# Optimization experiments

Measured on AMD Instinct MI355X. Metric: run time of the kernel, lower is better.

## Reference

```python
import jax, jax.numpy as jnp
import numpy as np

N_NODES = 50000
N_EDGES = 800000
H_DIM = 128
N_REL = 40
N_BASES = 4


def setup_inputs() -> dict:
    key = jax.random.key(0)
    ks = jax.random.split(key, 9)
    h = jax.random.normal(ks[0], (N_NODES, H_DIM), jnp.float32)
    norm = jax.random.uniform(ks[1], (N_EDGES, 1), jnp.float32)
    basis_w = jax.random.normal(ks[2], (N_BASES, H_DIM, H_DIM), jnp.float32) * 0.05
    w_comp = jax.random.normal(ks[3], (N_REL, N_BASES), jnp.float32) * 0.5
    loop_w = jax.random.normal(ks[4], (H_DIM, H_DIM), jnp.float32) * 0.05
    bias = jax.random.normal(ks[5], (H_DIM,), jnp.float32) * 0.05
    src = jax.random.randint(ks[6], (N_EDGES,), 0, N_NODES, jnp.int32)
    dst = jax.random.randint(ks[7], (N_EDGES,), 0, N_NODES, jnp.int32)
    etype = jax.random.randint(ks[8], (N_EDGES,), 0, N_REL, jnp.int32)
    return {"h": h, "norm": norm, "basis_w": basis_w, "w_comp": w_comp,
            "loop_w": loop_w, "bias": bias, "src": src, "dst": dst, "etype": etype}


def reference(h, norm, basis_w, w_comp, loop_w, bias, src, dst, etype):
    # RelGraphConv with 'basis' regularizer, one layer (num_hidden_layers=1):
    #   W_r = sum_b w_comp[r, b] * basis_w[b]
    #   m_e = (h[src_e] @ W_{etype_e}) * norm_e
    #   agg[v] = sum_{e: dst_e = v} m_e
    #   out = relu(agg + bias + h @ loop_w)   (dropout = 0)
    # Contraction reordered for memory efficiency: scatter-add per-basis
    # scaled source features first (node-level), then apply small basis GEMMs.
    n = h.shape[0]
    n_bases = basis_w.shape[0]
    coeff = w_comp[etype] * norm          # [E, B] per-edge basis coefficients * norm
    h_src = h[src]                        # [E, D] edge-gathered source features
    agg = jnp.zeros((n, basis_w.shape[2]), dtype=h.dtype)
    for b in range(n_bases):              # small fixed loop over bases
        s_b = jax.ops.segment_sum(coeff[:, b:b + 1] * h_src, dst, num_segments=n)  # [N, D]
        agg = agg + s_b @ basis_w[b]
    return jax.nn.relu(agg + bias + h @ loop_w)
```

## Files before the change

### kernel.cpp

```cpp
#include <hip/hip_runtime.h>
#include <hip/hip_bf16.h>
#include <stdint.h>

#define N_NODES 50000
#define N_EDGES 800000
#define H_DIM 128
#define N_REL 40
#define N_BASES 4
#define A_COLS 640
#define N_RANGES 196
#define EP_BLOCKS 200
#define EDGES_PER_BLK 4000
#define STAGE_CAP 5120

typedef __attribute__((ext_vector_type(8))) short bf16x8;
typedef __attribute__((ext_vector_type(4))) float f32x4;

__device__ __forceinline__ unsigned short f2bf(float f) {
    unsigned int u = __float_as_uint(f);
    unsigned int r = u + 0x7fffu + ((u >> 16) & 1u);
    return (unsigned short)(r >> 16);
}

__global__ __launch_bounds__(256) void prep_kernel(
        const float* __restrict__ h,
        const float* __restrict__ basis_w, const float* __restrict__ loop_w,
        const int* __restrict__ src, const int* __restrict__ dst,
        const int* __restrict__ etype, const float* __restrict__ norm,
        unsigned short* __restrict__ A, unsigned short* __restrict__ wt3,
        uint2* __restrict__ pkd, int* __restrict__ gcnt) {
    int bid = blockIdx.x;
    if (bid < 3125) {
        int t = bid * 256 + threadIdx.x;
        int row = t >> 4;
        int cb = (t & 15) * 8;
        const float* p = h + (size_t)row * 128 + cb;
        float4 a0 = ((const float4*)p)[0];
        float4 a1 = ((const float4*)p)[1];
        bf16x8 o;
        o[0] = (short)f2bf(a0.x); o[1] = (short)f2bf(a0.y);
        o[2] = (short)f2bf(a0.z); o[3] = (short)f2bf(a0.w);
        o[4] = (short)f2bf(a1.x); o[5] = (short)f2bf(a1.y);
        o[6] = (short)f2bf(a1.z); o[7] = (short)f2bf(a1.w);
        *(bf16x8*)(A + (size_t)row * A_COLS + cb) = o;
    } else if (bid < 3130) {
        int mat = bid - 3125;
        const float* srcm = (mat < 4) ? (basis_w + mat * 16384) : loop_w;
        int koff = (mat < 4) ? (128 + mat * 128) : 0;
        int t = threadIdx.x;
#pragma unroll
        for (int i = 0; i < 16; ++i) {
            int f = t + i * 256;
            int k = f >> 5;
            int j4 = (f & 31) * 4;
            float4 v = ((const float4*)srcm)[f];
            int kg = koff + k;
            int ks = kg >> 5;
            int quad = (kg >> 3) & 3;
            int jj = kg & 7;
            float vv[4] = {v.x, v.y, v.z, v.w};
#pragma unroll
            for (int d = 0; d < 4; ++d) {
                int j = j4 + d;
                int cg = j >> 4;
                int n16 = j & 15;
                wt3[(size_t)((ks * 8 + cg) * 64 + quad * 16 + n16) * 8 + jj] =
                    f2bf(vv[d]);
            }
        }
    } else {
        __shared__ int lhist[N_RANGES];
        int blk = bid - 3130;
        int t = threadIdx.x;
        if (t < N_RANGES) lhist[t] = 0;
        __syncthreads();
        int e0 = blk * EDGES_PER_BLK;
        for (int i = t; i < EDGES_PER_BLK; i += 256) {
            int e = e0 + i;
            int d = dst[e];
            unsigned int nbf = f2bf(norm[e]);
            pkd[e] = make_uint2((unsigned)src[e] | ((unsigned)etype[e] << 20),
                                (unsigned)d | (nbf << 17));
            atomicAdd(&lhist[d >> 8], 1);
        }
        __syncthreads();
        if (t < N_RANGES) gcnt[t * EP_BLOCKS + blk] = lhist[t];
    }
}

__global__ __launch_bounds__(256) void bucket_scan_a(
        const int* __restrict__ gcnt, int* __restrict__ blkbase,
        int* __restrict__ btot) {
    __shared__ int wsum[4];
    int r = blockIdx.x;
    int t = threadIdx.x, lane = t & 63, w = t >> 6;
    int x = (t < EP_BLOCKS) ? gcnt[r * EP_BLOCKS + t] : 0;
    int v = x;
#pragma unroll
    for (int d = 1; d < 64; d <<= 1) {
        int y = __shfl_up(v, d);
        if (lane >= d) v += y;
    }
    if (lane == 63) wsum[w] = v;
    __syncthreads();
    int wpre = 0;
    if (w > 0) wpre += wsum[0];
    if (w > 1) wpre += wsum[1];
    if (w > 2) wpre += wsum[2];
    if (t < EP_BLOCKS) blkbase[r * EP_BLOCKS + t] = wpre + v - x;
    if (t == 255) btot[r] = wpre + v;
}

__global__ __launch_bounds__(256) void bucket_scan_b(
        const int* __restrict__ btot, int* __restrict__ bstart,
        int* __restrict__ offs) {
    __shared__ int wsum[4];
    int t = threadIdx.x, lane = t & 63, w = t >> 6;
    int x = (t < N_RANGES) ? btot[t] : 0;
    int v = x;
#pragma unroll
    for (int d = 1; d < 64; d <<= 1) {
        int y = __shfl_up(v, d);
        if (lane >= d) v += y;
    }
    if (lane == 63) wsum[w] = v;
    __syncthreads();
    int wpre = 0;
    if (w > 0) wpre += wsum[0];
    if (w > 1) wpre += wsum[1];
    if (w > 2) wpre += wsum[2];
    if (t < N_RANGES) bstart[t] = wpre + v - x;
    if (t == 255) {
        bstart[N_RANGES] = wpre + v;
        offs[N_NODES] = wpre + v;
    }
}

__global__ __launch_bounds__(256) void binscatter(
        const uint2* __restrict__ pkd, const int* __restrict__ blkbase,
        const int* __restrict__ bstart, uint2* __restrict__ bucketed) {
    __shared__ int lcur[N_RANGES];
    int t = threadIdx.x;
    if (t < N_RANGES)
        lcur[t] = bstart[t] + blkbase[t * EP_BLOCKS + blockIdx.x];
    __syncthreads();
    int e0 = blockIdx.x * EDGES_PER_BLK;
    for (int i = t; i < EDGES_PER_BLK; i += 256) {
        uint2 p = pkd[e0 + i];
        int r = (p.y & 0x1FFFF) >> 8;
        int pos = atomicAdd(&lcur[r], 1);
        bucketed[pos] = p;
    }
}

__global__ __launch_bounds__(256) void bucket_sort(
        const int* __restrict__ bstart, const uint2* __restrict__ bucketed,
        uint2* __restrict__ sorted_pe, int* __restrict__ offs) {
    __shared__ int hist[256];
    __shared__ int cur[256];
    __shared__ int wsum[4];
    __shared__ uint2 stage[STAGE_CAP];
    int r = blockIdx.x;
    int t = threadIdx.x, lane = t & 63, w = t >> 6;
    int begin = bstart[r];
    int end = bstart[r + 1];
    int n = end - begin;
    hist[t] = 0;
    __syncthreads();
    for (int i = begin + t; i < end; i += 256)
        atomicAdd(&hist[bucketed[i].y & 255], 1);
    __syncthreads();
    int x = hist[t];
    int v = x;
#pragma unroll
    for (int d = 1; d < 64; d <<= 1) {
        int y = __shfl_up(v, d);
        if (lane >= d) v += y;
    }
    if (lane == 63) wsum[w] = v;
    __syncthreads();
    int wpre = 0;
    if (w > 0) wpre += wsum[0];
    if (w > 1) wpre += wsum[1];
    if (w > 2) wpre += wsum[2];
    int excl_rel = wpre + v - x;
    int node = r * 256 + t;
    if (node < N_NODES) offs[node] = begin + excl_rel;
    cur[t] = excl_rel;
    __syncthreads();
    if (n <= STAGE_CAP) {
        for (int i = begin + t; i < end; i += 256) {
            uint2 p = bucketed[i];
            int pos = atomicAdd(&cur[p.y & 255], 1);
            stage[pos] = make_uint2(p.x, (p.y >> 17) << 16);
        }
        __syncthreads();
        for (int i = t; i < n; i += 256)
            sorted_pe[begin + i] = stage[i];
    } else {
        for (int i = begin + t; i < end; i += 256) {
            uint2 p = bucketed[i];
            int pos = atomicAdd(&cur[p.y & 255], 1);
            sorted_pe[begin + pos] = make_uint2(p.x, (p.y >> 17) << 16);
        }
    }
}

__global__ __launch_bounds__(256) void aggregate_kernel(
        const int* __restrict__ offs, const uint2* __restrict__ sorted_pe,
        const float* __restrict__ w_comp,
        unsigned short* __restrict__ A) {
    int v = __builtin_amdgcn_readfirstlane(blockIdx.x * 4 + (threadIdx.x >> 6));
    if (v >= N_NODES) return;
    int lane = threadIdx.x & 63;
    int begin = offs[v];
    int end = offs[v + 1];

    float a0l = 0.f, a0h = 0.f, a1l = 0.f, a1h = 0.f;
    float a2l = 0.f, a2h = 0.f, a3l = 0.f, a3h = 0.f;

    const unsigned int* Au = (const unsigned int*)A;

    int j = begin;
    for (; j + 8 <= end; j += 8) {
        uint2 p[8];
        unsigned int u[8];
#pragma unroll
        for (int q = 0; q < 8; ++q) p[q] = sorted_pe[j + q];
#pragma unroll
        for (int q = 0; q < 8; ++q)
            u[q] = Au[(size_t)(p[q].x & 0xFFFFF) * 320 + lane];
#pragma unroll
        for (int q = 0; q < 8; ++q) {
            float4 wc = ((const float4*)w_comp)[p[q].x >> 20];
            float nm = __uint_as_float(p[q].y);
            float lo = __uint_as_float(u[q] << 16);
            float hi = __uint_as_float(u[q] & 0xffff0000u);
            a0l += (wc.x * nm) * lo; a0h += (wc.x * nm) * hi;
            a1l += (wc.y * nm) * lo; a1h += (wc.y * nm) * hi;
            a2l += (wc.z * nm) * lo; a2h += (wc.z * nm) * hi;
            a3l += (wc.w * nm) * lo; a3h += (wc.w * nm) * hi;
        }
    }
    for (; j < end; ++j) {
        uint2 p = sorted_pe[j];
        int s = p.x & 0xFFFFF;
        float4 wc = ((const float4*)w_comp)[p.x >> 20];
        float nm = __uint_as_float(p.y);
        unsigned int u = Au[(size_t)s * 320 + lane];
        float lo = __uint_as_float(u << 16);
        float hi = __uint_as_float(u & 0xffff0000u);
        a0l += (wc.x * nm) * lo; a0h += (wc.x * nm) * hi;
        a1l += (wc.y * nm) * lo; a1h += (wc.y * nm) * hi;
        a2l += (wc.z * nm) * lo; a2h += (wc.z * nm) * hi;
        a3l += (wc.w * nm) * lo; a3h += (wc.w * nm) * hi;
    }

    unsigned int* ps = (unsigned int*)(A + (size_t)v * A_COLS + 128);
    ps[0 * 64 + lane] = (unsigned int)f2bf(a0l) | ((unsigned int)f2bf(a0h) << 16);
    ps[1 * 64 + lane] = (unsigned int)f2bf(a1l) | ((unsigned int)f2bf(a1h) << 16);
    ps[2 * 64 + lane] = (unsigned int)f2bf(a2l) | ((unsigned int)f2bf(a2h) << 16);
    ps[3 * 64 + lane] = (unsigned int)f2bf(a3l) | ((unsigned int)f2bf(a3h) << 16);
}

__global__ __launch_bounds__(256, 2) void gemm_out(
        const unsigned short* __restrict__ A,
        const unsigned short* __restrict__ wt3,
        const float* __restrict__ bias,
        float* __restrict__ out) {
    int wv = threadIdx.x >> 6;
    int lane = threadIdx.x & 63;
    int n16 = lane & 15;
    int quad = lane >> 4;
    int r0 = (blockIdx.x * 4 + wv) * 32;

    const unsigned short* ap0 = A + (size_t)(r0 + n16) * A_COLS + quad * 8;
    const unsigned short* ap1 = ap0 + 16 * A_COLS;
    const unsigned short* bp = wt3 + (size_t)lane * 8;

    f32x4 acc[2][8];
#pragma unroll
    for (int rt = 0; rt < 2; ++rt)
#pragma unroll
        for (int ct = 0; ct < 8; ++ct)
            acc[rt][ct] = (f32x4)0.f;

    bf16x8 a_cur[2], b_cur[8];
    a_cur[0] = *(const bf16x8*)ap0;
    a_cur[1] = *(const bf16x8*)ap1;
#pragma unroll
    for (int ct = 0; ct < 8; ++ct)
        b_cur[ct] = *(const bf16x8*)(bp + ct * 512);

#pragma unroll
    for (int ks = 0; ks < 20; ++ks) {
        bf16x8 a_nxt[2], b_nxt[8];
        if (ks < 19) {
            a_nxt[0] = *(const bf16x8*)(ap0 + (ks + 1) * 32);
            a_nxt[1] = *(const bf16x8*)(ap1 + (ks + 1) * 32);
#pragma unroll
            for (int ct = 0; ct < 8; ++ct)
                b_nxt[ct] = *(const bf16x8*)(bp + (ks + 1) * 4096 + ct * 512);
        } else {
            a_nxt[0] = a_cur[0];
            a_nxt[1] = a_cur[1];
#pragma unroll
            for (int ct = 0; ct < 8; ++ct) b_nxt[ct] = b_cur[ct];
        }
#pragma unroll
        for (int ct = 0; ct < 8; ++ct) {
            acc[0][ct] = __builtin_amdgcn_mfma_f32_16x16x32_bf16(a_cur[0], b_cur[ct], acc[0][ct], 0, 0, 0);
            acc[1][ct] = __builtin_amdgcn_mfma_f32_16x16x32_bf16(a_cur[1], b_cur[ct], acc[1][ct], 0, 0, 0);
        }
        a_cur[0] = a_nxt[0];
        a_cur[1] = a_nxt[1];
#pragma unroll
        for (int ct = 0; ct < 8; ++ct) b_cur[ct] = b_nxt[ct];
    }

#pragma unroll
    for (int rt = 0; rt < 2; ++rt) {
        int rbase = r0 + rt * 16 + quad * 4;
#pragma unroll
        for (int ct = 0; ct < 8; ++ct) {
            int col = ct * 16 + n16;
            float bv = bias[col];
#pragma unroll
            for (int rg = 0; rg < 4; ++rg) {
                int r = rbase + rg;
                if (r < N_NODES)
                    out[(size_t)r * H_DIM + col] = fmaxf(acc[rt][ct][rg] + bv, 0.f);
            }
        }
    }
}

extern "C" void kernel_launch(void* const* d_in, const int* in_sizes, int n_in,
                              void* d_out, int out_size, void* d_ws, size_t ws_size,
                              hipStream_t stream) {
    const float* h       = (const float*)d_in[0];
    const float* norm    = (const float*)d_in[1];
    const float* basis_w = (const float*)d_in[2];
    const float* w_comp  = (const float*)d_in[3];
    const float* loop_w  = (const float*)d_in[4];
    const float* bias    = (const float*)d_in[5];
    const int*   src     = (const int*)d_in[6];
    const int*   dst     = (const int*)d_in[7];
    const int*   etype   = (const int*)d_in[8];
    float* out = (float*)d_out;

    char* base = (char*)d_ws;
    unsigned short* wt3       = (unsigned short*)(base + 0);
    unsigned short* A         = (unsigned short*)(base + 163840);
    int*            offs      = (int*)(base + 64225280);
    uint2*          pkd       = (uint2*)(base + 64425344);
    uint2*          bucketed  = (uint2*)(base + 70825344);
    uint2*          sorted_pe = (uint2*)(base + 77225344);
    int*            gcnt      = (int*)(base + 83625344);
    int*            blkbase   = (int*)(base + 83782144);
    int*            bstart    = (int*)(base + 83938944);
    int*            btot      = (int*)(base + 83939732);

    prep_kernel<<<3330, 256, 0, stream>>>(h, basis_w, loop_w,
                                          src, dst, etype, norm,
                                          A, wt3, pkd, gcnt);
    bucket_scan_a<<<N_RANGES, 256, 0, stream>>>(gcnt, blkbase, btot);
    bucket_scan_b<<<1, 256, 0, stream>>>(btot, bstart, offs);
    binscatter<<<EP_BLOCKS, 256, 0, stream>>>(pkd, blkbase, bstart, bucketed);
    bucket_sort<<<N_RANGES, 256, 0, stream>>>(bstart, bucketed, sorted_pe, offs);
    aggregate_kernel<<<12500, 256, 0, stream>>>(offs, sorted_pe, w_comp, A);
    gemm_out<<<391, 256, 0, stream>>>(A, wt3, bias, out);
}
```

Baseline: 199.2 us.

## Fuse aggregation into output GEMM via shared memory and fold bucket scan into consumers

Fuses the per-node aggregation kernel with the output GEMM. Each block aggregates 32 nodes into a swizzled LDS tile that feeds MFMA directly, so the 640-column bf16 intermediate is no longer written to and read back from global memory. The bf16 copy of h shrinks to 128 columns, and the single-block global scan is recomputed redundantly inside binscatter and bucket_sort, which removes two launches. The cost is 40KB of LDS per block, which lowers occupancy, and a per-block aggregation phase whose load imbalance can stall the MFMA phase.

```diff
diff --git a/kernel.cpp b/kernel.cpp
--- a/kernel.cpp
+++ b/kernel.cpp
@@ -1,5 +1,4 @@
 #include <hip/hip_runtime.h>
-#include <hip/hip_bf16.h>
 #include <stdint.h>
 
 #define N_NODES 50000
@@ -7,7 +6,6 @@
 #define H_DIM 128
 #define N_REL 40
 #define N_BASES 4
-#define A_COLS 640
 #define N_RANGES 196
 #define EP_BLOCKS 200
 #define EDGES_PER_BLK 4000
@@ -42,7 +40,7 @@
         o[2] = (short)f2bf(a0.z); o[3] = (short)f2bf(a0.w);
         o[4] = (short)f2bf(a1.x); o[5] = (short)f2bf(a1.y);
         o[6] = (short)f2bf(a1.z); o[7] = (short)f2bf(a1.w);
-        *(bf16x8*)(A + (size_t)row * A_COLS + cb) = o;
+        *(bf16x8*)(A + (size_t)row * H_DIM + cb) = o;
     } else if (bid < 3130) {
         int mat = bid - 3125;
         const float* srcm = (mat < 4) ? (basis_w + mat * 16384) : loop_w;
@@ -111,9 +109,10 @@
     if (t == 255) btot[r] = wpre + v;
 }
 
-__global__ __launch_bounds__(256) void bucket_scan_b(
-        const int* __restrict__ btot, int* __restrict__ bstart,
-        int* __restrict__ offs) {
+__global__ __launch_bounds__(256) void binscatter(
+        const uint2* __restrict__ pkd, const int* __restrict__ blkbase,
+        const int* __restrict__ btot, uint2* __restrict__ bucketed) {
+    __shared__ int lcur[N_RANGES];
     __shared__ int wsum[4];
     int t = threadIdx.x, lane = t & 63, w = t >> 6;
     int x = (t < N_RANGES) ? btot[t] : 0;
@@ -129,20 +128,8 @@
     if (w > 0) wpre += wsum[0];
     if (w > 1) wpre += wsum[1];
     if (w > 2) wpre += wsum[2];
-    if (t < N_RANGES) bstart[t] = wpre + v - x;
-    if (t == 255) {
-        bstart[N_RANGES] = wpre + v;
-        offs[N_NODES] = wpre + v;
-    }
-}
-
-__global__ __launch_bounds__(256) void binscatter(
-        const uint2* __restrict__ pkd, const int* __restrict__ blkbase,
-        const int* __restrict__ bstart, uint2* __restrict__ bucketed) {
-    __shared__ int lcur[N_RANGES];
-    int t = threadIdx.x;
     if (t < N_RANGES)
-        lcur[t] = bstart[t] + blkbase[t * EP_BLOCKS + blockIdx.x];
+        lcur[t] = (wpre + v - x) + blkbase[t * EP_BLOCKS + blockIdx.x];
     __syncthreads();
     int e0 = blockIdx.x * EDGES_PER_BLK;
     for (int i = t; i < EDGES_PER_BLK; i += 256) {
@@ -154,23 +141,16 @@
 }
 
 __global__ __launch_bounds__(256) void bucket_sort(
-        const int* __restrict__ bstart, const uint2* __restrict__ bucketed,
+        const int* __restrict__ btot, const uint2* __restrict__ bucketed,
         uint2* __restrict__ sorted_pe, int* __restrict__ offs) {
     __shared__ int hist[256];
     __shared__ int cur[256];
     __shared__ int wsum[4];
+    __shared__ int sbeg;
     __shared__ uint2 stage[STAGE_CAP];
     int r = blockIdx.x;
     int t = threadIdx.x, lane = t & 63, w = t >> 6;
-    int begin = bstart[r];
-    int end = bstart[r + 1];
-    int n = end - begin;
-    hist[t] = 0;
-    __syncthreads();
-    for (int i = begin + t; i < end; i += 256)
-        atomicAdd(&hist[bucketed[i].y & 255], 1);
-    __syncthreads();
-    int x = hist[t];
+    int x = (t < N_RANGES) ? btot[t] : 0;
     int v = x;
 #pragma unroll
     for (int d = 1; d < 64; d <<= 1) {
@@ -178,14 +158,37 @@
         if (lane >= d) v += y;
     }
     if (lane == 63) wsum[w] = v;
+    hist[t] = 0;
     __syncthreads();
     int wpre = 0;
     if (w > 0) wpre += wsum[0];
     if (w > 1) wpre += wsum[1];
     if (w > 2) wpre += wsum[2];
-    int excl_rel = wpre + v - x;
+    if (t == r) sbeg = wpre + v - x;
+    __syncthreads();
+    int begin = sbeg;
+    int end = begin + btot[r];
+    int n = end - begin;
+    for (int i = begin + t; i < end; i += 256)
+        atomicAdd(&hist[bucketed[i].y & 255], 1);
+    __syncthreads();
+    int x2 = hist[t];
+    int v2 = x2;
+#pragma unroll
+    for (int d = 1; d < 64; d <<= 1) {
+        int y = __shfl_up(v2, d);
+        if (lane >= d) v2 += y;
+    }
+    if (lane == 63) wsum[w] = v2;
+    __syncthreads();
+    int wpre2 = 0;
+    if (w > 0) wpre2 += wsum[0];
+    if (w > 1) wpre2 += wsum[1];
+    if (w > 2) wpre2 += wsum[2];
+    int excl_rel = wpre2 + v2 - x2;
     int node = r * 256 + t;
     if (node < N_NODES) offs[node] = begin + excl_rel;
+    if (r == N_RANGES - 1 && t == 0) offs[N_NODES] = N_EDGES;
     cur[t] = excl_rel;
     __syncthreads();
     if (n <= STAGE_CAP) {
@@ -206,130 +209,113 @@
     }
 }
 
-__global__ __launch_bounds__(256) void aggregate_kernel(
+__global__ __launch_bounds__(256) void agg_gemm(
         const int* __restrict__ offs, const uint2* __restrict__ sorted_pe,
         const float* __restrict__ w_comp,
-        unsigned short* __restrict__ A) {
-    int v = __builtin_amdgcn_readfirstlane(blockIdx.x * 4 + (threadIdx.x >> 6));
-    if (v >= N_NODES) return;
-    int lane = threadIdx.x & 63;
-    int begin = offs[v];
-    int end = offs[v + 1];
-
-    float a0l = 0.f, a0h = 0.f, a1l = 0.f, a1h = 0.f;
-    float a2l = 0.f, a2h = 0.f, a3l = 0.f, a3h = 0.f;
-
-    const unsigned int* Au = (const unsigned int*)A;
-
-    int j = begin;
-    for (; j + 8 <= end; j += 8) {
-        uint2 p[8];
-        unsigned int u[8];
-#pragma unroll
-        for (int q = 0; q < 8; ++q) p[q] = sorted_pe[j + q];
-#pragma unroll
-        for (int q = 0; q < 8; ++q)
-            u[q] = Au[(size_t)(p[q].x & 0xFFFFF) * 320 + lane];
-#pragma unroll
-        for (int q = 0; q < 8; ++q) {
-            float4 wc = ((const float4*)w_comp)[p[q].x >> 20];
-            float nm = __uint_as_float(p[q].y);
-            float lo = __uint_as_float(u[q] << 16);
-            float hi = __uint_as_float(u[q] & 0xffff0000u);
-            a0l += (wc.x * nm) * lo; a0h += (wc.x * nm) * hi;
-            a1l += (wc.y * nm) * lo; a1h += (wc.y * nm) * hi;
-            a2l += (wc.z * nm) * lo; a2h += (wc.z * nm) * hi;
-            a3l += (wc.w * nm) * lo; a3h += (wc.w * nm) * hi;
-        }
-    }
-    for (; j < end; ++j) {
-        uint2 p = sorted_pe[j];
-        int s = p.x & 0xFFFFF;
-        float4 wc = ((const float4*)w_comp)[p.x >> 20];
-        float nm = __uint_as_float(p.y);
-        unsigned int u = Au[(size_t)s * 320 + lane];
-        float lo = __uint_as_float(u << 16);
-        float hi = __uint_as_float(u & 0xffff0000u);
-        a0l += (wc.x * nm) * lo; a0h += (wc.x * nm) * hi;
-        a1l += (wc.y * nm) * lo; a1h += (wc.y * nm) * hi;
-        a2l += (wc.z * nm) * lo; a2h += (wc.z * nm) * hi;
-        a3l += (wc.w * nm) * lo; a3h += (wc.w * nm) * hi;
-    }
-
-    unsigned int* ps = (unsigned int*)(A + (size_t)v * A_COLS + 128);
-    ps[0 * 64 + lane] = (unsigned int)f2bf(a0l) | ((unsigned int)f2bf(a0h) << 16);
-    ps[1 * 64 + lane] = (unsigned int)f2bf(a1l) | ((unsigned int)f2bf(a1h) << 16);
-    ps[2 * 64 + lane] = (unsigned int)f2bf(a2l) | ((unsigned int)f2bf(a2h) << 16);
-    ps[3 * 64 + lane] = (unsigned int)f2bf(a3l) | ((unsigned int)f2bf(a3h) << 16);
-}
-
-__global__ __launch_bounds__(256, 2) void gemm_out(
-        const unsigned short* __restrict__ A,
+        const unsigned short* __restrict__ Ab,
         const unsigned short* __restrict__ wt3,
-        const float* __restrict__ bias,
-        float* __restrict__ out) {
+        const float* __restrict__ bias, float* __restrict__ out) {
+    __shared__ __align__(16) unsigned short S[32 * 640];
     int wv = threadIdx.x >> 6;
     int lane = threadIdx.x & 63;
+    int nbase = blockIdx.x * 32;
+    const unsigned int* Au = (const unsigned int*)Ab;
+
+    for (int q = 0; q < 8; ++q) {
+        int row = (wv << 3) + q;
+        int v = __builtin_amdgcn_readfirstlane(nbase + row);
+        float a0l = 0.f, a0h = 0.f, a1l = 0.f, a1h = 0.f;
+        float a2l = 0.f, a2h = 0.f, a3l = 0.f, a3h = 0.f;
+        unsigned int hb = 0u;
+        if (v < N_NODES) {
+            hb = Au[(size_t)v * 64 + lane];
+            int begin = offs[v];
+            int end = offs[v + 1];
+            int j = begin;
+            for (; j + 8 <= end; j += 8) {
+                uint2 p[8];
+                unsigned int u[8];
+#pragma unroll
+                for (int k = 0; k < 8; ++k) p[k] = sorted_pe[j + k];
+#pragma unroll
+                for (int k = 0; k < 8; ++k)
+                    u[k] = Au[(size_t)(p[k].x & 0xFFFFF) * 64 + lane];
+#pragma unroll
+                for (int k = 0; k < 8; ++k) {
+                    float4 wc = ((const float4*)w_comp)[p[k].x >> 20];
+                    float nm = __uint_as_float(p[k].y);
+                    float lo = __uint_as_float(u[k] << 16);
+                    float hi = __uint_as_float(u[k] & 0xffff0000u);
+                    a0l += (wc.x * nm) * lo; a0h += (wc.x * nm) * hi;
+                    a1l += (wc.y * nm) * lo; a1h += (wc.y * nm) * hi;
+                    a2l += (wc.z * nm) * lo; a2h += (wc.z * nm) * hi;
+                    a3l += (wc.w * nm) * lo; a3h += (wc.w * nm) * hi;
+                }
+            }
+            for (; j < end; ++j) {
+                uint2 p = sorted_pe[j];
+                float4 wc = ((const float4*)w_comp)[p.x >> 20];
+                float nm = __uint_as_float(p.y);
+                unsigned int u = Au[(size_t)(p.x & 0xFFFFF) * 64 + lane];
+                float lo = __uint_as_float(u << 16);
+                float hi = __uint_as_float(u & 0xffff0000u);
+                a0l += (wc.x * nm) * lo; a0h += (wc.x * nm) * hi;
+                a1l += (wc.y * nm) * lo; a1h += (wc.y * nm) * hi;
+                a2l += (wc.z * nm) * lo; a2h += (wc.z * nm) * hi;
+                a3l += (wc.w * nm) * lo; a3h += (wc.w * nm) * hi;
+            }
+        }
+        char* rp = (char*)S + row * 1280;
+        int swz = (row & 7) << 4;
+        *(unsigned int*)(rp + ((lane * 4) ^ swz)) = hb;
+        *(unsigned int*)(rp + ((256 + lane * 4) ^ swz)) =
+            (unsigned int)f2bf(a0l) | ((unsigned int)f2bf(a0h) << 16);
+        *(unsigned int*)(rp + ((512 + lane * 4) ^ swz)) =
+            (unsigned int)f2bf(a1l) | ((unsigned int)f2bf(a1h) << 16);
+        *(unsigned int*)(rp + ((768 + lane * 4) ^ swz)) =
+            (unsigned int)f2bf(a2l) | ((unsigned int)f2bf(a2h) << 16);
+        *(unsigned int*)(rp + ((1024 + lane * 4) ^ swz)) =
+            (unsigned int)f2bf(a3l) | ((unsigned int)f2bf(a3h) << 16);
+    }
+    __syncthreads();
+
     int n16 = lane & 15;
     int quad = lane >> 4;
-    int r0 = (blockIdx.x * 4 + wv) * 32;
-
-    const unsigned short* ap0 = A + (size_t)(r0 + n16) * A_COLS + quad * 8;
-    const unsigned short* ap1 = ap0 + 16 * A_COLS;
-    const unsigned short* bp = wt3 + (size_t)lane * 8;
-
-    f32x4 acc[2][8];
+    f32x4 acc[2][2];
 #pragma unroll
     for (int rt = 0; rt < 2; ++rt)
 #pragma unroll
-        for (int ct = 0; ct < 8; ++ct)
-            acc[rt][ct] = (f32x4)0.f;
-
-    bf16x8 a_cur[2], b_cur[8];
-    a_cur[0] = *(const bf16x8*)ap0;
-    a_cur[1] = *(const bf16x8*)ap1;
-#pragma unroll
-    for (int ct = 0; ct < 8; ++ct)
-        b_cur[ct] = *(const bf16x8*)(bp + ct * 512);
+        for (int c = 0; c < 2; ++c) acc[rt][c] = (f32x4)0.f;
+
+    const char* a0p = (const char*)S + n16 * 1280;
+    const char* a1p = (const char*)S + (16 + n16) * 1280;
+    int swz2 = (n16 & 7) << 4;
+    const unsigned short* bp = wt3 + (size_t)(wv * 2) * 512 + lane * 8;
 
 #pragma unroll
     for (int ks = 0; ks < 20; ++ks) {
-        bf16x8 a_nxt[2], b_nxt[8];
-        if (ks < 19) {
-            a_nxt[0] = *(const bf16x8*)(ap0 + (ks + 1) * 32);
-            a_nxt[1] = *(const bf16x8*)(ap1 + (ks + 1) * 32);
-#pragma unroll
-            for (int ct = 0; ct < 8; ++ct)
-                b_nxt[ct] = *(const bf16x8*)(bp + (ks + 1) * 4096 + ct * 512);
-        } else {
-            a_nxt[0] = a_cur[0];
-            a_nxt[1] = a_cur[1];
-#pragma unroll
-            for (int ct = 0; ct < 8; ++ct) b_nxt[ct] = b_cur[ct];
-        }
-#pragma unroll
-        for (int ct = 0; ct < 8; ++ct) {
-            acc[0][ct] = __builtin_amdgcn_mfma_f32_16x16x32_bf16(a_cur[0], b_cur[ct], acc[0][ct], 0, 0, 0);
-            acc[1][ct] = __builtin_amdgcn_mfma_f32_16x16x32_bf16(a_cur[1], b_cur[ct], acc[1][ct], 0, 0, 0);
-        }
-        a_cur[0] = a_nxt[0];
-        a_cur[1] = a_nxt[1];
-#pragma unroll
-        for (int ct = 0; ct < 8; ++ct) b_cur[ct] = b_nxt[ct];
+        int off = (ks * 64 + quad * 16) ^ swz2;
+        bf16x8 a0 = *(const bf16x8*)(a0p + off);
+        bf16x8 a1 = *(const bf16x8*)(a1p + off);
+        bf16x8 b0 = *(const bf16x8*)(bp + (size_t)ks * 4096);
+        bf16x8 b1 = *(const bf16x8*)(bp + (size_t)ks * 4096 + 512);
+        acc[0][0] = __builtin_amdgcn_mfma_f32_16x16x32_bf16(a0, b0, acc[0][0], 0, 0, 0);
+        acc[1][0] = __builtin_amdgcn_mfma_f32_16x16x32_bf16(a1, b0, acc[1][0], 0, 0, 0);
+        acc[0][1] = __builtin_amdgcn_mfma_f32_16x16x32_bf16(a0, b1, acc[0][1], 0, 0, 0);
+        acc[1][1] = __builtin_amdgcn_mfma_f32_16x16x32_bf16(a1, b1, acc[1][1], 0, 0, 0);
     }
 
 #pragma unroll
     for (int rt = 0; rt < 2; ++rt) {
-        int rbase = r0 + rt * 16 + quad * 4;
-#pragma unroll
-        for (int ct = 0; ct < 8; ++ct) {
-            int col = ct * 16 + n16;
+#pragma unroll
+        for (int c = 0; c < 2; ++c) {
+            int col = (wv * 2 + c) * 16 + n16;
             float bv = bias[col];
 #pragma unroll
             for (int rg = 0; rg < 4; ++rg) {
-                int r = rbase + rg;
+                int r = nbase + rt * 16 + quad * 4 + rg;
                 if (r < N_NODES)
-                    out[(size_t)r * H_DIM + col] = fmaxf(acc[rt][ct][rg] + bv, 0.f);
+                    out[(size_t)r * H_DIM + col] = fmaxf(acc[rt][c][rg] + bv, 0.f);
             }
         }
     }
@@ -352,22 +338,19 @@
     char* base = (char*)d_ws;
     unsigned short* wt3       = (unsigned short*)(base + 0);
     unsigned short* A         = (unsigned short*)(base + 163840);
-    int*            offs      = (int*)(base + 64225280);
-    uint2*          pkd       = (uint2*)(base + 64425344);
-    uint2*          bucketed  = (uint2*)(base + 70825344);
-    uint2*          sorted_pe = (uint2*)(base + 77225344);
-    int*            gcnt      = (int*)(base + 83625344);
-    int*            blkbase   = (int*)(base + 83782144);
-    int*            bstart    = (int*)(base + 83938944);
-    int*            btot      = (int*)(base + 83939732);
+    int*            offs      = (int*)(base + 12963840);
+    uint2*          pkd       = (uint2*)(base + 13163848);
+    uint2*          bucketed  = (uint2*)(base + 19563848);
+    uint2*          sorted_pe = (uint2*)(base + 25963848);
+    int*            gcnt      = (int*)(base + 32363848);
+    int*            blkbase   = (int*)(base + 32520648);
+    int*            btot      = (int*)(base + 32677448);
 
     prep_kernel<<<3330, 256, 0, stream>>>(h, basis_w, loop_w,
                                           src, dst, etype, norm,
                                           A, wt3, pkd, gcnt);
     bucket_scan_a<<<N_RANGES, 256, 0, stream>>>(gcnt, blkbase, btot);
-    bucket_scan_b<<<1, 256, 0, stream>>>(btot, bstart, offs);
-    binscatter<<<EP_BLOCKS, 256, 0, stream>>>(pkd, blkbase, bstart, bucketed);
-    bucket_sort<<<N_RANGES, 256, 0, stream>>>(bstart, bucketed, sorted_pe, offs);
-    aggregate_kernel<<<12500, 256, 0, stream>>>(offs, sorted_pe, w_comp, A);
-    gemm_out<<<391, 256, 0, stream>>>(A, wt3, bias, out);
-}
+    binscatter<<<EP_BLOCKS, 256, 0, stream>>>(pkd, blkbase, btot, bucketed);
+    bucket_sort<<<N_RANGES, 256, 0, stream>>>(btot, bucketed, sorted_pe, offs);
+    agg_gemm<<<1563, 256, 0, stream>>>(offs, sorted_pe, w_comp, A, wt3, bias, out);
+}
```

Measured after the change: 193.3 us. 1.03x faster.
